# Kernel optimization log

Hardware: AMD Instinct MI355X
Metric: run time of the kernel (lower is better)

The kernel has to match this reference:

```python
import jax, jax.numpy as jnp
import numpy as np

N_NODES = 50000
N_EDGES = 800000
IN_FEATS = 128
N_HIDDEN = 64
OUT_FEATS = 40
DIM = 8  # pseudo-coordinate dimension
K = 1    # n_kernels


def setup_inputs() -> dict:
    key = jax.random.key(0)
    ks = jax.random.split(key, 12)
    inp = {
        "features": jax.random.normal(ks[0], (N_NODES, IN_FEATS), dtype=jnp.float32),
        "edge_weight": jax.random.normal(ks[1], (N_EDGES, DIM), dtype=jnp.float32),
        "src": jax.random.randint(ks[2], (N_EDGES,), 0, N_NODES),
        "dst": jax.random.randint(ks[3], (N_EDGES,), 0, N_NODES),
        # layer 1 params (fc has no bias in DGL GMMConv; separate additive bias)
        "W1": jax.random.normal(ks[4], (IN_FEATS, K * N_HIDDEN), dtype=jnp.float32) * (1.0 / np.sqrt(IN_FEATS)),
        "b1": jnp.zeros((N_HIDDEN,), dtype=jnp.float32),
        "mu1": jax.random.normal(ks[5], (K, DIM), dtype=jnp.float32) * 0.1,
        "inv_sigma1": jnp.ones((K, DIM), dtype=jnp.float32),
        # layer 2 params
        "W2": jax.random.normal(ks[6], (N_HIDDEN, K * OUT_FEATS), dtype=jnp.float32) * (1.0 / np.sqrt(N_HIDDEN)),
        "b2": jnp.zeros((OUT_FEATS,), dtype=jnp.float32),
        "mu2": jax.random.normal(ks[7], (K, DIM), dtype=jnp.float32) * 0.1,
        "inv_sigma2": jnp.ones((K, DIM), dtype=jnp.float32),
    }
    return inp


def gmm_conv(x, pseudo, src, dst, W, b, mu, inv_sigma, out_feats):
    # x: [N, in], pseudo: [E, DIM], W: [in, K*out]
    h = (x @ W).reshape(-1, K, out_feats)                      # [N, K, out]
    # gaussian mixture weights per edge/kernel: [E, K]
    diff = pseudo[:, None, :] - mu[None, :, :]                 # [E, K, DIM]
    gw = jnp.exp(-0.5 * jnp.sum(diff * diff * (inv_sigma[None] ** 2), axis=-1))
    # gather src feats, weight, sum over kernels: [E, out]
    msg = jnp.einsum("ekf,ek->ef", h[src], gw)
    agg = jax.ops.segment_sum(msg, dst, num_segments=N_NODES)  # [N, out]
    return agg + b


def reference(features, edge_weight, src, dst, W1, b1, mu1, inv_sigma1, W2, b2, mu2, inv_sigma2):
    x = gmm_conv(features, edge_weight, src, dst, W1, b1, mu1, inv_sigma1, N_HIDDEN)
    x = gmm_conv(x, edge_weight, src, dst, W2, b2, mu2, inv_sigma2, OUT_FEATS)
    return jax.nn.log_softmax(x, axis=1)
```

## Files before the change

kernel.cpp:

```cpp
#include <hip/hip_runtime.h>
#include <hip/hip_fp16.h>
#include <math.h>

#define N_NODES 50000
#define N_EDGES 800000
#define IN_FEATS 128
#define N_HIDDEN 64
#define OUT_FEATS 40
#define DIM 8
#define GT_TILES ((N_NODES + 63) / 64)
#define HIST_NB ((N_EDGES / 4 + 255) / 256)
#define FILL_BLOCKS (N_EDGES / 256)
#define SCAN_NB ((N_NODES + 255) / 256)
#define CNT_STRIDE 4
#define WCOLS 48
#define W12_NB ((WCOLS * IN_FEATS) / 256)

typedef _Float16 half8 __attribute__((ext_vector_type(8)));
typedef float floatx4 __attribute__((ext_vector_type(4)));

__device__ __forceinline__ int wave_incl_scan(int x, int lane) {
#pragma unroll
    for (int off = 1; off < 64; off <<= 1) {
        int v = __shfl_up(x, off, 64);
        if (lane >= off) x += v;
    }
    return x;
}

__global__ __launch_bounds__(256) void w12_kernel(const float* __restrict__ W1,
                                                  const float* __restrict__ W2,
                                                  const float* __restrict__ b1,
                                                  __half* __restrict__ w12T,
                                                  float* __restrict__ cvec) {
    const int idx = blockIdx.x * 256 + threadIdx.x;
    const int c = idx >> 7;
    const int i = idx & 127;
    float s = 0.f;
    if (c < OUT_FEATS) {
#pragma unroll 8
        for (int k = 0; k < N_HIDDEN; ++k)
            s += W1[i * N_HIDDEN + k] * W2[k * OUT_FEATS + c];
    }
    w12T[idx] = __float2half(s);
    if (idx < OUT_FEATS) {
        float t = 0.f;
        for (int k = 0; k < N_HIDDEN; ++k)
            t += b1[k] * W2[k * OUT_FEATS + idx];
        cvec[idx] = t;
    }
}

__global__ __launch_bounds__(256) void histgemm_kernel(
    const float* __restrict__ features, const __half* __restrict__ w12T,
    const int* __restrict__ dst,
    int* __restrict__ counts, unsigned short* __restrict__ rank,
    __half* __restrict__ y)
{
    const int tid = threadIdx.x;
    __shared__ __align__(16) __half WT[WCOLS][136];

    if (blockIdx.x < HIST_NB) {
        int i = blockIdx.x * 256 + tid;
        if (i * 4 >= N_EDGES) return;
        int4 d = ((const int4*)dst)[i];
        ushort4 r;
        r.x = (unsigned short)atomicAdd(&counts[d.x * CNT_STRIDE], 1);
        r.y = (unsigned short)atomicAdd(&counts[d.y * CNT_STRIDE], 1);
        r.z = (unsigned short)atomicAdd(&counts[d.z * CNT_STRIDE], 1);
        r.w = (unsigned short)atomicAdd(&counts[d.w * CNT_STRIDE], 1);
        ((ushort4*)rank)[i] = r;
        return;
    }

    int nodeBase = (blockIdx.x - HIST_NB) * 64;
    for (int rep = 0; rep < (WCOLS * IN_FEATS) / 256; ++rep) {
        int idx = tid + rep * 256;
        WT[idx >> 7][idx & 127] = w12T[idx];
    }
    __syncthreads();

    int lane = tid & 63, w = tid >> 6;
    int m = lane & 15, quad = lane >> 4;
    int row = nodeBase + w * 16 + m;
    int rowc = (row < N_NODES) ? row : (N_NODES - 1);
    const float* fr = features + (size_t)rowc * IN_FEATS;

    floatx4 acc0 = {0.f,0.f,0.f,0.f}, acc1 = acc0, acc2 = acc0;
#pragma unroll
    for (int kc = 0; kc < 4; ++kc) {
        float4 fa = *(const float4*)(fr + kc * 32 + quad * 8);
        float4 fb = *(const float4*)(fr + kc * 32 + quad * 8 + 4);
        union { half8 v; __half2 h2[4]; } A;
        A.h2[0] = __floats2half2_rn(fa.x, fa.y);
        A.h2[1] = __floats2half2_rn(fa.z, fa.w);
        A.h2[2] = __floats2half2_rn(fb.x, fb.y);
        A.h2[3] = __floats2half2_rn(fb.z, fb.w);
        half8 b0 = *(const half8*)&WT[ 0 + m][kc * 32 + quad * 8];
        half8 b1 = *(const half8*)&WT[16 + m][kc * 32 + quad * 8];
        half8 b2 = *(const half8*)&WT[32 + m][kc * 32 + quad * 8];
        acc0 = __builtin_amdgcn_mfma_f32_16x16x32_f16(A.v, b0, acc0, 0, 0, 0);
        acc1 = __builtin_amdgcn_mfma_f32_16x16x32_f16(A.v, b1, acc1, 0, 0, 0);
        acc2 = __builtin_amdgcn_mfma_f32_16x16x32_f16(A.v, b2, acc2, 0, 0, 0);
    }
    int nodeRow = nodeBase + w * 16 + quad * 4;
#pragma unroll
    for (int r = 0; r < 4; ++r) {
        int n = nodeRow + r;
        if (n < N_NODES) {
            size_t base = (size_t)n * OUT_FEATS;
            y[base + m]      = __float2half(acc0[r]);
            y[base + m + 16] = __float2half(acc1[r]);
            if (m < 8)
                y[base + m + 32] = __float2half(acc2[r]);
        }
    }
}

__global__ __launch_bounds__(256) void scan_partial_kernel(const int* __restrict__ counts,
                                                           int* __restrict__ offsets,
                                                           int* __restrict__ partials) {
    const int tid = threadIdx.x, bid = blockIdx.x;
    const int i = bid * 256 + tid;
    const int lane = tid & 63, wid = tid >> 6;
    int x = (i < N_NODES) ? counts[i * CNT_STRIDE] : 0;
    int incl = wave_incl_scan(x, lane);
    __shared__ int wsum[4];
    if (lane == 63) wsum[wid] = incl;
    __syncthreads();
    int base = 0;
#pragma unroll
    for (int w = 0; w < 4; ++w)
        if (w < wid) base += wsum[w];
    if (i < N_NODES) offsets[i] = base + incl - x;
    if (tid == 255) partials[bid] = base + incl;
}

__global__ __launch_bounds__(256) void scan_base_kernel(int* __restrict__ partials) {
    const int tid = threadIdx.x;
    const int lane = tid & 63, wid = tid >> 6;
    int x = (tid < SCAN_NB) ? partials[tid] : 0;
    int incl = wave_incl_scan(x, lane);
    __shared__ int wsum[4];
    if (lane == 63) wsum[wid] = incl;
    __syncthreads();
    int base = 0;
#pragma unroll
    for (int w = 0; w < 4; ++w)
        if (w < wid) base += wsum[w];
    if (tid < SCAN_NB) partials[tid] = base + incl - x;
}

__global__ __launch_bounds__(256) void scan_add_kernel(int* __restrict__ offsets,
                                                       const int* __restrict__ partials) {
    const int i = blockIdx.x * 256 + threadIdx.x;
    if (i < N_NODES) offsets[i] += partials[blockIdx.x];
    if (i == N_NODES) offsets[N_NODES] = N_EDGES;
}

__global__ __launch_bounds__(256) void fill_kernel(
    const int* __restrict__ src, const int* __restrict__ dst,
    const float* __restrict__ ew,
    const float* __restrict__ mu1, const float* __restrict__ is1,
    const float* __restrict__ mu2, const float* __restrict__ is2,
    const int* __restrict__ offsets, const unsigned short* __restrict__ rank,
    int2* __restrict__ csr)
{
    int e = blockIdx.x * 256 + threadIdx.x;
    int sN = src[e];
    int dN = dst[e];
    unsigned short rk = rank[e];
    const float4* ew4 = (const float4*)(ew + (size_t)e * DIM);
    float4 wa = ew4[0], wb = ew4[1];
    float v[8] = {wa.x, wa.y, wa.z, wa.w, wb.x, wb.y, wb.z, wb.w};
    float s1 = 0.f, s2 = 0.f;
#pragma unroll
    for (int d = 0; d < DIM; ++d) {
        float d1 = v[d] - mu1[d]; float a1 = is1[d];
        float d2 = v[d] - mu2[d]; float a2 = is2[d];
        s1 += d1 * d1 * a1 * a1;
        s2 += d2 * d2 * a2 * a2;
    }
    __half2 g = __floats2half2_rn(expf(-0.5f * s1), expf(-0.5f * s2));
    int2 rec;
    rec.x = sN;
    rec.y = *reinterpret_cast<int*>(&g);
    int pos = offsets[dN] + rk;
    __builtin_nontemporal_store(*reinterpret_cast<long long*>(&rec),
                                reinterpret_cast<long long*>(&csr[pos]));
}

__global__ __launch_bounds__(256) void agg1_kernel(const __half* __restrict__ ysrc,
                                                   const int* __restrict__ offsets,
                                                   const int2* __restrict__ csr,
                                                   const float* __restrict__ cvec,
                                                   __half* __restrict__ h2) {
    const unsigned* h32 = (const unsigned*)ysrc;
    const int tid = threadIdx.x;
    const int w = tid >> 6, lane = tid & 63;
    const int hf = lane >> 5, p = lane & 31;
    const int n = blockIdx.x * 8 + w * 2 + hf;
    const int pc = (p < 20) ? p : 19;
    int beg = offsets[n], end = offsets[n + 1];

    float ax = 0.f, ay = 0.f;
    for (int j = beg; j < end; j += 8) {
        int j0 = j + 0, j1 = j + 1, j2 = j + 2, j3 = j + 3;
        int j4 = j + 4, j5 = j + 5, j6 = j + 6, j7 = j + 7;
        int e1 = end - 1;
        int2 r0 = csr[(j0 < end) ? j0 : e1];
        int2 r1 = csr[(j1 < end) ? j1 : e1];
        int2 r2 = csr[(j2 < end) ? j2 : e1];
        int2 r3 = csr[(j3 < end) ? j3 : e1];
        int2 r4 = csr[(j4 < end) ? j4 : e1];
        int2 r5 = csr[(j5 < end) ? j5 : e1];
        int2 r6 = csr[(j6 < end) ? j6 : e1];
        int2 r7 = csr[(j7 < end) ? j7 : e1];
        unsigned v0 = h32[(size_t)r0.x * 20 + pc];
        unsigned v1 = h32[(size_t)r1.x * 20 + pc];
        unsigned v2 = h32[(size_t)r2.x * 20 + pc];
        unsigned v3 = h32[(size_t)r3.x * 20 + pc];
        unsigned v4 = h32[(size_t)r4.x * 20 + pc];
        unsigned v5 = h32[(size_t)r5.x * 20 + pc];
        unsigned v6 = h32[(size_t)r6.x * 20 + pc];
        unsigned v7 = h32[(size_t)r7.x * 20 + pc];
        float g0 = (j0 < end) ? __low2float(*reinterpret_cast<__half2*>(&r0.y)) : 0.f;
        float g1 = (j1 < end) ? __low2float(*reinterpret_cast<__half2*>(&r1.y)) : 0.f;
        float g2 = (j2 < end) ? __low2float(*reinterpret_cast<__half2*>(&r2.y)) : 0.f;
        float g3 = (j3 < end) ? __low2float(*reinterpret_cast<__half2*>(&r3.y)) : 0.f;
        float g4 = (j4 < end) ? __low2float(*reinterpret_cast<__half2*>(&r4.y)) : 0.f;
        float g5 = (j5 < end) ? __low2float(*reinterpret_cast<__half2*>(&r5.y)) : 0.f;
        float g6 = (j6 < end) ? __low2float(*reinterpret_cast<__half2*>(&r6.y)) : 0.f;
        float g7 = (j7 < end) ? __low2float(*reinterpret_cast<__half2*>(&r7.y)) : 0.f;
        float2 f0 = __half22float2(*reinterpret_cast<__half2*>(&v0));
        float2 f1 = __half22float2(*reinterpret_cast<__half2*>(&v1));
        float2 f2 = __half22float2(*reinterpret_cast<__half2*>(&v2));
        float2 f3 = __half22float2(*reinterpret_cast<__half2*>(&v3));
        float2 f4 = __half22float2(*reinterpret_cast<__half2*>(&v4));
        float2 f5 = __half22float2(*reinterpret_cast<__half2*>(&v5));
        float2 f6 = __half22float2(*reinterpret_cast<__half2*>(&v6));
        float2 f7 = __half22float2(*reinterpret_cast<__half2*>(&v7));
        ax += f0.x * g0; ay += f0.y * g0;
        ax += f1.x * g1; ay += f1.y * g1;
        ax += f2.x * g2; ay += f2.y * g2;
        ax += f3.x * g3; ay += f3.y * g3;
        ax += f4.x * g4; ay += f4.y * g4;
        ax += f5.x * g5; ay += f5.y * g5;
        ax += f6.x * g6; ay += f6.y * g6;
        ax += f7.x * g7; ay += f7.y * g7;
    }
    if (p < 20) {
        __half2 hv = __floats2half2_rn(ax + cvec[2 * p], ay + cvec[2 * p + 1]);
        ((unsigned*)h2)[(size_t)n * 20 + p] = *reinterpret_cast<unsigned*>(&hv);
    }
}

__global__ __launch_bounds__(256) void agg2_kernel(const __half* __restrict__ h,
                                                   const int* __restrict__ offsets,
                                                   const int2* __restrict__ csr,
                                                   const float* __restrict__ b,
                                                   float* __restrict__ out) {
    const unsigned* h32 = (const unsigned*)h;
    const int tid = threadIdx.x;
    const int w = tid >> 6, lane = tid & 63;
    const int hf = lane >> 5, p = lane & 31;
    const int n = blockIdx.x * 8 + w * 2 + hf;
    const int pc = (p < 20) ? p : 19;
    int beg = offsets[n], end = offsets[n + 1];

    float ax = 0.f, ay = 0.f;
    for (int j = beg; j < end; j += 8) {
        int j0 = j + 0, j1 = j + 1, j2 = j + 2, j3 = j + 3;
        int j4 = j + 4, j5 = j + 5, j6 = j + 6, j7 = j + 7;
        int e1 = end - 1;
        int2 r0 = csr[(j0 < end) ? j0 : e1];
        int2 r1 = csr[(j1 < end) ? j1 : e1];
        int2 r2 = csr[(j2 < end) ? j2 : e1];
        int2 r3 = csr[(j3 < end) ? j3 : e1];
        int2 r4 = csr[(j4 < end) ? j4 : e1];
        int2 r5 = csr[(j5 < end) ? j5 : e1];
        int2 r6 = csr[(j6 < end) ? j6 : e1];
        int2 r7 = csr[(j7 < end) ? j7 : e1];
        unsigned v0 = h32[(size_t)r0.x * 20 + pc];
        unsigned v1 = h32[(size_t)r1.x * 20 + pc];
        unsigned v2 = h32[(size_t)r2.x * 20 + pc];
        unsigned v3 = h32[(size_t)r3.x * 20 + pc];
        unsigned v4 = h32[(size_t)r4.x * 20 + pc];
        unsigned v5 = h32[(size_t)r5.x * 20 + pc];
        unsigned v6 = h32[(size_t)r6.x * 20 + pc];
        unsigned v7 = h32[(size_t)r7.x * 20 + pc];
        float g0 = (j0 < end) ? __high2float(*reinterpret_cast<__half2*>(&r0.y)) : 0.f;
        float g1 = (j1 < end) ? __high2float(*reinterpret_cast<__half2*>(&r1.y)) : 0.f;
        float g2 = (j2 < end) ? __high2float(*reinterpret_cast<__half2*>(&r2.y)) : 0.f;
        float g3 = (j3 < end) ? __high2float(*reinterpret_cast<__half2*>(&r3.y)) : 0.f;
        float g4 = (j4 < end) ? __high2float(*reinterpret_cast<__half2*>(&r4.y)) : 0.f;
        float g5 = (j5 < end) ? __high2float(*reinterpret_cast<__half2*>(&r5.y)) : 0.f;
        float g6 = (j6 < end) ? __high2float(*reinterpret_cast<__half2*>(&r6.y)) : 0.f;
        float g7 = (j7 < end) ? __high2float(*reinterpret_cast<__half2*>(&r7.y)) : 0.f;
        float2 f0 = __half22float2(*reinterpret_cast<__half2*>(&v0));
        float2 f1 = __half22float2(*reinterpret_cast<__half2*>(&v1));
        float2 f2 = __half22float2(*reinterpret_cast<__half2*>(&v2));
        float2 f3 = __half22float2(*reinterpret_cast<__half2*>(&v3));
        float2 f4 = __half22float2(*reinterpret_cast<__half2*>(&v4));
        float2 f5 = __half22float2(*reinterpret_cast<__half2*>(&v5));
        float2 f6 = __half22float2(*reinterpret_cast<__half2*>(&v6));
        float2 f7 = __half22float2(*reinterpret_cast<__half2*>(&v7));
        ax += f0.x * g0; ay += f0.y * g0;
        ax += f1.x * g1; ay += f1.y * g1;
        ax += f2.x * g2; ay += f2.y * g2;
        ax += f3.x * g3; ay += f3.y * g3;
        ax += f4.x * g4; ay += f4.y * g4;
        ax += f5.x * g5; ay += f5.y * g5;
        ax += f6.x * g6; ay += f6.y * g6;
        ax += f7.x * g7; ay += f7.y * g7;
    }

    bool valid = (p < 20);
    float vx = valid ? ax + b[2 * p]     : -INFINITY;
    float vy = valid ? ay + b[2 * p + 1] : -INFINITY;
    float m = fmaxf(vx, vy);
#pragma unroll
    for (int off = 16; off; off >>= 1)
        m = fmaxf(m, __shfl_xor(m, off, 32));
    float ex = valid ? (expf(vx - m) + expf(vy - m)) : 0.f;
#pragma unroll
    for (int off = 16; off; off >>= 1)
        ex += __shfl_xor(ex, off, 32);
    float ls = logf(ex);
    if (valid) {
        float2 o = make_float2(vx - m - ls, vy - m - ls);
        *(float2*)&out[(size_t)n * OUT_FEATS + 2 * p] = o;
    }
}

extern "C" void kernel_launch(void* const* d_in, const int* in_sizes, int n_in,
                              void* d_out, int out_size, void* d_ws, size_t ws_size,
                              hipStream_t stream) {
    const float* features    = (const float*)d_in[0];
    const float* edge_weight = (const float*)d_in[1];
    const int*   src         = (const int*)d_in[2];
    const int*   dst         = (const int*)d_in[3];
    const float* W1          = (const float*)d_in[4];
    const float* b1          = (const float*)d_in[5];
    const float* mu1         = (const float*)d_in[6];
    const float* is1         = (const float*)d_in[7];
    const float* W2          = (const float*)d_in[8];
    const float* b2          = (const float*)d_in[9];
    const float* mu2         = (const float*)d_in[10];
    const float* is2         = (const float*)d_in[11];
    float* out = (float*)d_out;

    int2*           csr     = (int2*)d_ws;
    __half*         Y       = (__half*)(csr + N_EDGES);
    __half*         h2      = Y + (size_t)N_NODES * OUT_FEATS;
    int*            counts  = (int*)(h2 + (size_t)N_NODES * OUT_FEATS);
    unsigned short* rank    = (unsigned short*)(counts + N_NODES * CNT_STRIDE);
    int*            offsets = (int*)(rank + N_EDGES);
    int*            partials= offsets + N_NODES + 1;
    __half*         w12T    = (__half*)(partials + 256);
    float*          cvec    = (float*)(w12T + WCOLS * IN_FEATS);

    hipMemsetAsync(counts, 0, (size_t)N_NODES * CNT_STRIDE * sizeof(int), stream);

    w12_kernel<<<W12_NB, 256, 0, stream>>>(W1, W2, b1, w12T, cvec);

    histgemm_kernel<<<HIST_NB + GT_TILES, 256, 0, stream>>>(
        features, w12T, dst, counts, rank, Y);

    scan_partial_kernel<<<SCAN_NB, 256, 0, stream>>>(counts, offsets, partials);
    scan_base_kernel<<<1, 256, 0, stream>>>(partials);
    scan_add_kernel<<<SCAN_NB, 256, 0, stream>>>(offsets, partials);

    fill_kernel<<<FILL_BLOCKS, 256, 0, stream>>>(
        src, dst, edge_weight, mu1, is1, mu2, is2, offsets, rank, csr);

    agg1_kernel<<<N_NODES / 8, 256, 0, stream>>>(Y, offsets, csr, cvec, h2);

    agg2_kernel<<<N_NODES / 8, 256, 0, stream>>>(h2, offsets, csr, b2, out);
}
```

Before: 226.2 us.

## Fuse three-pass scan into single-pass decoupled look-back and fold memset

Replaces the three-kernel prefix scan over per-node edge counts with one kernel that uses decoupled look-back: each block publishes its aggregate or inclusive prefix into a flag-tagged partials array and spins on its predecessors. It also moves zeroing of the counts and partials buffers into the weight-precompute kernel, dropping a separate memset. The goal is to cut launch and serialization overhead between small kernels. In exchange it relies on blocks being scheduled in index order to avoid deadlock, and the serial look-back chain may add latency.

```diff
diff --git a/kernel.cpp b/kernel.cpp
--- a/kernel.cpp
+++ b/kernel.cpp
@@ -32,22 +32,29 @@
                                                   const float* __restrict__ W2,
                                                   const float* __restrict__ b1,
                                                   __half* __restrict__ w12T,
-                                                  float* __restrict__ cvec) {
-    const int idx = blockIdx.x * 256 + threadIdx.x;
-    const int c = idx >> 7;
-    const int i = idx & 127;
+                                                  float* __restrict__ cvec,
+                                                  int* __restrict__ counts,
+                                                  int* __restrict__ partials) {
+    const int gtid = blockIdx.x * 256 + threadIdx.x;
+
+    for (int i = gtid; i < (N_NODES * CNT_STRIDE) / 4; i += W12_NB * 256)
+        ((int4*)counts)[i] = make_int4(0, 0, 0, 0);
+    if (gtid < 256) partials[gtid] = 0;
+
+    const int c = gtid >> 7;
+    const int i = gtid & 127;
     float s = 0.f;
     if (c < OUT_FEATS) {
 #pragma unroll 8
         for (int k = 0; k < N_HIDDEN; ++k)
             s += W1[i * N_HIDDEN + k] * W2[k * OUT_FEATS + c];
     }
-    w12T[idx] = __float2half(s);
-    if (idx < OUT_FEATS) {
+    w12T[gtid] = __float2half(s);
+    if (gtid < OUT_FEATS) {
         float t = 0.f;
         for (int k = 0; k < N_HIDDEN; ++k)
-            t += b1[k] * W2[k * OUT_FEATS + idx];
-        cvec[idx] = t;
+            t += b1[k] * W2[k * OUT_FEATS + gtid];
+        cvec[gtid] = t;
     }
 }
 
@@ -117,45 +124,51 @@
     }
 }
 
-__global__ __launch_bounds__(256) void scan_partial_kernel(const int* __restrict__ counts,
-                                                           int* __restrict__ offsets,
-                                                           int* __restrict__ partials) {
+__global__ __launch_bounds__(256) void scan_kernel(const int* __restrict__ counts,
+                                                   int* __restrict__ offsets,
+                                                   int* __restrict__ partials) {
     const int tid = threadIdx.x, bid = blockIdx.x;
     const int i = bid * 256 + tid;
     const int lane = tid & 63, wid = tid >> 6;
     int x = (i < N_NODES) ? counts[i * CNT_STRIDE] : 0;
     int incl = wave_incl_scan(x, lane);
     __shared__ int wsum[4];
+    __shared__ int sExc, sTot;
     if (lane == 63) wsum[wid] = incl;
     __syncthreads();
     int base = 0;
 #pragma unroll
     for (int w = 0; w < 4; ++w)
         if (w < wid) base += wsum[w];
-    if (i < N_NODES) offsets[i] = base + incl - x;
-    if (tid == 255) partials[bid] = base + incl;
-}
-
-__global__ __launch_bounds__(256) void scan_base_kernel(int* __restrict__ partials) {
-    const int tid = threadIdx.x;
-    const int lane = tid & 63, wid = tid >> 6;
-    int x = (tid < SCAN_NB) ? partials[tid] : 0;
-    int incl = wave_incl_scan(x, lane);
-    __shared__ int wsum[4];
-    if (lane == 63) wsum[wid] = incl;
+    int lexcl = base + incl - x;
+    if (tid == 255) sTot = base + incl;
     __syncthreads();
-    int base = 0;
-#pragma unroll
-    for (int w = 0; w < 4; ++w)
-        if (w < wid) base += wsum[w];
-    if (tid < SCAN_NB) partials[tid] = base + incl - x;
-}
-
-__global__ __launch_bounds__(256) void scan_add_kernel(int* __restrict__ offsets,
-                                                       const int* __restrict__ partials) {
-    const int i = blockIdx.x * 256 + threadIdx.x;
-    if (i < N_NODES) offsets[i] += partials[blockIdx.x];
-    if (i == N_NODES) offsets[N_NODES] = N_EDGES;
+    if (tid == 0) {
+        int T = sTot;
+        if (bid == 0) {
+            __hip_atomic_store(&partials[0], (T << 2) | 2,
+                               __ATOMIC_RELAXED, __HIP_MEMORY_SCOPE_AGENT);
+            sExc = 0;
+        } else {
+            __hip_atomic_store(&partials[bid], (T << 2) | 1,
+                               __ATOMIC_RELAXED, __HIP_MEMORY_SCOPE_AGENT);
+            int sum = 0, pb = bid - 1;
+            while (true) {
+                int v = __hip_atomic_load(&partials[pb],
+                                          __ATOMIC_RELAXED, __HIP_MEMORY_SCOPE_AGENT);
+                if (v == 0) continue;
+                sum += v >> 2;
+                if ((v & 3) == 2) break;
+                --pb;
+            }
+            __hip_atomic_store(&partials[bid], ((sum + T) << 2) | 2,
+                               __ATOMIC_RELAXED, __HIP_MEMORY_SCOPE_AGENT);
+            sExc = sum;
+        }
+    }
+    __syncthreads();
+    if (i < N_NODES) offsets[i] = sExc + lexcl;
+    if (bid == SCAN_NB - 1 && tid == 0) offsets[N_NODES] = N_EDGES;
 }
 
 __global__ __launch_bounds__(256) void fill_kernel(
@@ -360,16 +373,12 @@
     __half*         w12T    = (__half*)(partials + 256);
     float*          cvec    = (float*)(w12T + WCOLS * IN_FEATS);
 
-    hipMemsetAsync(counts, 0, (size_t)N_NODES * CNT_STRIDE * sizeof(int), stream);
-
-    w12_kernel<<<W12_NB, 256, 0, stream>>>(W1, W2, b1, w12T, cvec);
+    w12_kernel<<<W12_NB, 256, 0, stream>>>(W1, W2, b1, w12T, cvec, counts, partials);
 
     histgemm_kernel<<<HIST_NB + GT_TILES, 256, 0, stream>>>(
         features, w12T, dst, counts, rank, Y);
 
-    scan_partial_kernel<<<SCAN_NB, 256, 0, stream>>>(counts, offsets, partials);
-    scan_base_kernel<<<1, 256, 0, stream>>>(partials);
-    scan_add_kernel<<<SCAN_NB, 256, 0, stream>>>(offsets, partials);
+    scan_kernel<<<SCAN_NB, 256, 0, stream>>>(counts, offsets, partials);
 
     fill_kernel<<<FILL_BLOCKS, 256, 0, stream>>>(
         src, dst, edge_weight, mu1, is1, mu2, is2, offsets, rank, csr);
```

Result: slower. 230.8 us (+2.1%).
